# Kernel optimization log

Measured on AMD Instinct MI355X. Metric: run time of the kernel, lower is better.

Reference implementation:

```python
import jax, jax.numpy as jnp
import numpy as np

N, T, C = 4, 2048, 1024
H = 16
D = C // H  # head_dim = 64


def setup_inputs() -> dict:
    key = jax.random.key(0)
    ks = jax.random.split(key, 6)
    s = 1.0 / np.sqrt(C)
    return {
        "x": jax.random.normal(ks[0], (N, T, C), dtype=jnp.float32),
        "Wq": jax.random.normal(ks[1], (C, C), dtype=jnp.float32) * s,
        "Wk": jax.random.normal(ks[2], (C, C), dtype=jnp.float32) * s,
        "Wv": jax.random.normal(ks[3], (C, C), dtype=jnp.float32) * s,
        "Wo": jax.random.normal(ks[4], (C, C), dtype=jnp.float32) * s,
        "bo": jax.random.normal(ks[5], (C,), dtype=jnp.float32) * s,
    }


def reference(x, Wq, Wk, Wv, Wo, bo):
    n, t, c = x.shape
    # torch nn.Linear: y = x @ W.T
    q = (x @ Wq.T).reshape(n, t, H, D).transpose(0, 2, 1, 3)  # [N,H,T,D]
    k = (x @ Wk.T).reshape(n, t, H, D).transpose(0, 2, 1, 3)
    v = (x @ Wv.T).reshape(n, t, H, D).transpose(0, 2, 1, 3)
    # NOTE: module scales by sqrt(embed_dim), not sqrt(head_dim)
    energy = jnp.einsum("nhqd,nhkd->nhqk", q, k) / jnp.sqrt(jnp.float32(c))
    causal = jnp.tril(jnp.ones((t, t), dtype=bool))  # [T,T]
    energy = jnp.where(causal[None, None], energy, -jnp.inf)
    attn = jax.nn.softmax(energy, axis=-1)
    out = jnp.einsum("nhqk,nhkd->nhqd", attn, v)  # [N,H,T,D]
    out = out.transpose(0, 2, 1, 3).reshape(n, t, c)
    return out @ Wo.T + bo
```

## Files before the change

### kernel.cpp

```cpp
#include <hip/hip_runtime.h>
#include <math.h>

#define N_ 4
#define T_ 2048
#define C_ 1024
#define H_ 16
#define D_ 64
#define NTC (N_*T_*C_)
#define WELEM (C_*C_)

typedef float f32x4  __attribute__((ext_vector_type(4)));
typedef float f32x16 __attribute__((ext_vector_type(16)));
typedef short bf16x8 __attribute__((ext_vector_type(8)));

static __device__ __forceinline__ unsigned short f2bf(float f) {
    union { float f; unsigned u; } v; v.f = f;
    unsigned r = v.u + 0x7FFFu + ((v.u >> 16) & 1u);
    return (unsigned short)(r >> 16);
}

static __device__ __forceinline__ unsigned cvtpk(float lo, float hi) {
    unsigned r;
    asm("v_cvt_pk_bf16_f32 %0, %1, %2" : "=v"(r) : "v"(lo), "v"(hi));
    return r;
}
#define PLSWAP(a, b) asm("v_permlane32_swap_b32 %0, %1" : "+v"(a), "+v"(b))

#define GLDS16(gptr, lptr) \
    __builtin_amdgcn_global_load_lds((const __attribute__((address_space(1))) void*)(gptr), \
                                     (__attribute__((address_space(3))) void*)(lptr), 16, 0, 0)

__global__ __launch_bounds__(256) void cast_x(const float* __restrict__ src,
                                              unsigned short* __restrict__ dst) {
    const int i = blockIdx.x * 256 + threadIdx.x;
    const float4 a = ((const float4*)src)[i * 2];
    const float4 b = ((const float4*)src)[i * 2 + 1];
    unsigned short u[8] = {f2bf(a.x), f2bf(a.y), f2bf(a.z), f2bf(a.w),
                           f2bf(b.x), f2bf(b.y), f2bf(b.z), f2bf(b.w)};
    *(uint4*)&dst[(size_t)i * 8] = *(const uint4*)u;
}

__global__ __launch_bounds__(256) void cast_w4(const float* __restrict__ w0,
                                               const float* __restrict__ w1,
                                               const float* __restrict__ w2,
                                               const float* __restrict__ w3,
                                               unsigned short* __restrict__ dst) {
    const int z = blockIdx.y;
    const float* __restrict__ src = (z == 0) ? w0 : (z == 1) ? w1 : (z == 2) ? w2 : w3;
    unsigned short* __restrict__ d = dst + (size_t)z * WELEM;
    const int i = blockIdx.x * 256 + threadIdx.x;
    const float4 a = ((const float4*)src)[i * 2];
    const float4 b = ((const float4*)src)[i * 2 + 1];
    unsigned short u[8] = {f2bf(a.x), f2bf(a.y), f2bf(a.z), f2bf(a.w),
                           f2bf(b.x), f2bf(b.y), f2bf(b.z), f2bf(b.w)};
    *(uint4*)&d[(size_t)i * 8] = *(const uint4*)u;
}

#define GEMM_BODY(Aptr, Bptr)                                                           \
    __shared__ __align__(16) unsigned short Abuf[128 * 32];                             \
    __shared__ __align__(16) unsigned short Bbuf[128 * 32];                             \
    const int tid  = threadIdx.x;                                                       \
    const int lane = tid & 63;                                                          \
    const int w    = tid >> 6;                                                          \
    const int lo   = lane & 15;                                                         \
    const int hi   = lane >> 4;                                                         \
    const int wm   = w >> 1;                                                            \
    const int wn   = w & 1;                                                             \
    const int rowBase = blockIdx.x * 128;                                               \
    const int colBase = blockIdx.y * 128;                                               \
    f32x4 acc[4][4];                                                                    \
    _Pragma("unroll")                                                                   \
    for (int i = 0; i < 4; ++i)                                                         \
        _Pragma("unroll")                                                               \
        for (int j = 0; j < 4; ++j) acc[i][j] = (f32x4)(0.f);                           \
    const int i0 = tid, i1 = tid + 256;                                                 \
    const int r0 = i0 >> 2, s0_ = i0 & 3, g0 = s0_ ^ ((r0 >> 1) & 3);                   \
    const int r1 = i1 >> 2, s1_ = i1 & 3, g1 = s1_ ^ ((r1 >> 1) & 3);                   \
    const unsigned short* gA0 = (Aptr) + (size_t)(rowBase + r0) * C_ + g0 * 8;          \
    const unsigned short* gA1 = (Aptr) + (size_t)(rowBase + r1) * C_ + g1 * 8;          \
    const unsigned short* gB0 = (Bptr) + (size_t)(colBase + r0) * C_ + g0 * 8;          \
    const unsigned short* gB1 = (Bptr) + (size_t)(colBase + r1) * C_ + g1 * 8;          \
    for (int k0 = 0; k0 < C_; k0 += 32) {                                               \
        GLDS16(gA0 + k0, &Abuf[i0 * 8]);                                                \
        GLDS16(gA1 + k0, &Abuf[i1 * 8]);                                                \
        GLDS16(gB0 + k0, &Bbuf[i0 * 8]);                                                \
        GLDS16(gB1 + k0, &Bbuf[i1 * 8]);                                                \
        __syncthreads();                                                                \
        bf16x8 af[4], bfv[4];                                                           \
        _Pragma("unroll")                                                               \
        for (int mi = 0; mi < 4; ++mi) {                                                \
            const int row = wm * 64 + mi * 16 + lo;                                     \
            const int slot = hi ^ ((row >> 1) & 3);                                     \
            af[mi] = *(const bf16x8*)&Abuf[row * 32 + slot * 8];                        \
        }                                                                               \
        _Pragma("unroll")                                                               \
        for (int ni = 0; ni < 4; ++ni) {                                                \
            const int row = wn * 64 + ni * 16 + lo;                                     \
            const int slot = hi ^ ((row >> 1) & 3);                                     \
            bfv[ni] = *(const bf16x8*)&Bbuf[row * 32 + slot * 8];                       \
        }                                                                               \
        _Pragma("unroll")                                                               \
        for (int mi = 0; mi < 4; ++mi)                                                  \
            _Pragma("unroll")                                                           \
            for (int ni = 0; ni < 4; ++ni)                                              \
                acc[mi][ni] = __builtin_amdgcn_mfma_f32_16x16x32_bf16(af[mi], bfv[ni],  \
                                                                     acc[mi][ni], 0, 0, 0); \
        __syncthreads();                                                                \
    }

__global__ __launch_bounds__(256) void qkv_fused(const unsigned short* __restrict__ A,
                                                 const unsigned short* __restrict__ Wall,
                                                 unsigned short* __restrict__ qkvout) {
    const int z = blockIdx.z;
    const unsigned short* __restrict__ B = Wall + (size_t)z * WELEM;
    unsigned short* __restrict__ Y = qkvout + (size_t)z * NTC;
    const float oscale = (z == 0) ? (0.03125f * 1.44269504f) : 1.0f;

    GEMM_BODY(A, B)

    if (z < 2) {
        #pragma unroll
        for (int mi = 0; mi < 4; ++mi) {
            #pragma unroll
            for (int r = 0; r < 4; ++r) {
                const int row = rowBase + wm * 64 + mi * 16 + hi * 4 + r;
                const int nn = row >> 11, tt = row & (T_ - 1);
                #pragma unroll
                for (int ni = 0; ni < 4; ++ni) {
                    const int col = colBase + wn * 64 + ni * 16 + lo;
                    Y[((size_t)((nn * H_ + (col >> 6)) * T_ + tt)) * D_ + (col & 63)] =
                        f2bf(acc[mi][ni][r] * oscale);
                }
            }
        }
    } else {
        #pragma unroll
        for (int mi = 0; mi < 4; ++mi) {
            #pragma unroll
            for (int r = 0; r < 4; ++r) {
                const int row = rowBase + wm * 64 + mi * 16 + hi * 4 + r;
                const int nn = row >> 11, tt = row & (T_ - 1);
                #pragma unroll
                for (int ni = 0; ni < 4; ++ni) {
                    const int col = colBase + wn * 64 + ni * 16 + lo;
                    Y[(size_t)((nn * 16 + (col >> 6)) * 64 + (col & 63)) * T_ + tt] =
                        f2bf(acc[mi][ni][r]);
                }
            }
        }
    }
}

__global__ __launch_bounds__(256) void out_gemm(const unsigned short* __restrict__ A,
                                                const unsigned short* __restrict__ B,
                                                const float* __restrict__ bo,
                                                float* __restrict__ out) {
    GEMM_BODY(A, B)

    float bias[4];
    #pragma unroll
    for (int ni = 0; ni < 4; ++ni) bias[ni] = bo[colBase + wn * 64 + ni * 16 + lo];
    #pragma unroll
    for (int mi = 0; mi < 4; ++mi) {
        #pragma unroll
        for (int r = 0; r < 4; ++r) {
            const int row = rowBase + wm * 64 + mi * 16 + hi * 4 + r;
            #pragma unroll
            for (int ni = 0; ni < 4; ++ni) {
                const int col = colBase + wn * 64 + ni * 16 + lo;
                out[(size_t)row * C_ + col] = acc[mi][ni][r] + bias[ni];
            }
        }
    }
}

__global__ __launch_bounds__(256, 2) void attn_mfma(const unsigned short* __restrict__ qg,
                                                    const unsigned short* __restrict__ kg,
                                                    const unsigned short* __restrict__ vtg,
                                                    unsigned short* __restrict__ ob) {
    __shared__ __align__(16) unsigned short Kt[2][64 * 64];
    __shared__ __align__(16) unsigned short Vt[2][64 * 64];

    const int tid  = threadIdx.x;
    const int w    = tid >> 6;
    const int lane = tid & 63;
    const int ql   = lane & 31;
    const int h    = lane >> 5;
    const int bid  = blockIdx.x;
    const int qtile = 15 - (bid >> 6);
    const int nh   = bid & 63;
    const int qb   = qtile * 128;
    const size_t base  = (size_t)nh * (T_ * D_);
    const size_t vbase = (size_t)nh * 64 * T_;
    const int qrow0 = qb + w * 32;

    bf16x8 qf[4];
    #pragma unroll
    for (int dsl = 0; dsl < 4; ++dsl)
        qf[dsl] = *(const bf16x8*)(qg + base + (size_t)(qrow0 + ql) * D_ + dsl * 16 + h * 8);

    f32x16 acc0 = (f32x16)(0.f), acc1 = (f32x16)(0.f);
    float mrun = -INFINITY, lrun = 0.f;

    const int mynkt  = (qrow0 >> 6) + 1;
    const int nktmax = (qb >> 6) + 2;
    const int csubdiag = (w & 1) + 1;

    const int i0 = tid, i1 = tid + 256;
    const int kr0 = i0 >> 3, kc0 = ((i0 & 7) ^ (kr0 & 7)) * 8;
    const int kr1 = i1 >> 3, kc1 = ((i1 & 7) ^ (kr1 & 7)) * 8;

    #define STAGE(kt_, buf_)                                                            \
        do {                                                                            \
            const int kb_ = (kt_) * 64;                                                 \
            GLDS16(kg + base + (size_t)(kb_ + kr0) * D_ + kc0, &Kt[buf_][i0 * 8]);      \
            GLDS16(kg + base + (size_t)(kb_ + kr1) * D_ + kc1, &Kt[buf_][i1 * 8]);      \
            GLDS16(vtg + vbase + (size_t)kr0 * T_ + kb_ + kc0, &Vt[buf_][i0 * 8]);      \
            GLDS16(vtg + vbase + (size_t)kr1 * T_ + kb_ + kc1, &Vt[buf_][i1 * 8]);      \
        } while (0)

    STAGE(0, 0);
    __syncthreads();
    int cur = 0;

    for (int kt = 0; kt < nktmax; ++kt) {
        if (kt + 1 < nktmax) STAGE(kt + 1, cur ^ 1);

        if (kt < mynkt) {
            const bool diag = (kt == mynkt - 1);
            const int csub = diag ? csubdiag : 2;
            const unsigned short* Kb = Kt[cur];
            const unsigned short* Vb = Vt[cur];

            f32x16 s0, s1;
            __builtin_amdgcn_s_setprio(1);
            {
                f32x16 z = (f32x16)(0.f);
                #pragma unroll
                for (int dsl = 0; dsl < 4; ++dsl) {
                    const bf16x8 ka = *(const bf16x8*)&Kb[ql * 64 + ((dsl * 2 + h) ^ (ql & 7)) * 8];
                    z = __builtin_amdgcn_mfma_f32_32x32x16_bf16(ka, qf[dsl], z, 0, 0, 0);
                }
                s0 = z;
            }
            if (csub > 1) {
                f32x16 z = (f32x16)(0.f);
                #pragma unroll
                for (int dsl = 0; dsl < 4; ++dsl) {
                    const bf16x8 ka = *(const bf16x8*)&Kb[(32 + ql) * 64 + ((dsl * 2 + h) ^ (ql & 7)) * 8];
                    z = __builtin_amdgcn_mfma_f32_32x32x16_bf16(ka, qf[dsl], z, 0, 0, 0);
                }
                s1 = z;
            }
            __builtin_amdgcn_s_setprio(0);

            if (diag) {
                #pragma unroll
                for (int r = 0; r < 16; ++r) {
                    const int rc = (r & 3) + 8 * (r >> 2) + 4 * h;
                    if (csub == 1) { if (rc > ql) s0[r] = -1e30f; }
                    else           { if (rc > ql) s1[r] = -1e30f; }
                }
            }

            float tm = fmaxf(s0[0], s0[1]);
            #pragma unroll
            for (int r = 2; r < 16; r += 2) tm = fmaxf(tm, fmaxf(s0[r], s0[r + 1]));
            if (csub > 1) {
                #pragma unroll
                for (int r = 0; r < 16; r += 2) tm = fmaxf(tm, fmaxf(s1[r], s1[r + 1]));
            }
            tm = fmaxf(tm, __shfl_xor(tm, 32));

            if (!__all(tm <= mrun + 8.f)) {
                const float mnew = fmaxf(mrun, tm);
                const float fsc = exp2f(mrun - mnew);
                mrun = mnew;
                lrun *= fsc;
                #pragma unroll
                for (int r = 0; r < 16; ++r) {
                    const float f = __shfl(fsc, (r & 3) + 8 * (r >> 2) + 4 * h);
                    acc0[r] *= f; acc1[r] *= f;
                }
            }

            float psum = 0.f;
            #pragma unroll
            for (int r = 0; r < 16; ++r) { s0[r] = exp2f(s0[r] - mrun); psum += s0[r]; }
            if (csub > 1) {
                #pragma unroll
                for (int r = 0; r < 16; ++r) { s1[r] = exp2f(s1[r] - mrun); psum += s1[r]; }
            }
            psum += __shfl_xor(psum, 32);
            lrun += psum;

            bf16x8 pa[4];
            #pragma unroll
            for (int a = 0; a < 2; ++a) {
                if (a < csub) {
                    #pragma unroll
                    for (int b = 0; b < 2; ++b) {
                        const f32x16& P = a ? s1 : s0;
                        unsigned w0 = cvtpk(P[8 * b + 0], P[8 * b + 1]);
                        unsigned w1 = cvtpk(P[8 * b + 2], P[8 * b + 3]);
                        unsigned w2 = cvtpk(P[8 * b + 4], P[8 * b + 5]);
                        unsigned w3 = cvtpk(P[8 * b + 6], P[8 * b + 7]);
                        PLSWAP(w0, w2);
                        PLSWAP(w1, w3);
                        unsigned wd[4] = {w0, w1, w2, w3};
                        pa[2 * a + b] = *(bf16x8*)wd;
                    }
                }
            }

            __builtin_amdgcn_s_setprio(1);
            #pragma unroll
            for (int ks = 0; ks < 4; ++ks) {
                if (ks < 2 * csub) {
                    const bf16x8 vf0 = *(const bf16x8*)&Vb[ql * 64 + ((ks * 2 + h) ^ (ql & 7)) * 8];
                    const bf16x8 vf1 = *(const bf16x8*)&Vb[(32 + ql) * 64 + ((ks * 2 + h) ^ (ql & 7)) * 8];
                    acc0 = __builtin_amdgcn_mfma_f32_32x32x16_bf16(pa[ks], vf0, acc0, 0, 0, 0);
                    acc1 = __builtin_amdgcn_mfma_f32_32x32x16_bf16(pa[ks], vf1, acc1, 0, 0, 0);
                }
            }
            __builtin_amdgcn_s_setprio(0);
        }
        __syncthreads();
        cur ^= 1;
    }

    const float linv = 1.f / lrun;
    const int nn = nh >> 4, hh = nh & 15;
    #pragma unroll
    for (int r = 0; r < 16; ++r) {
        const int rc = (r & 3) + 8 * (r >> 2) + 4 * h;
        const float li = __shfl(linv, rc);
        const size_t rb = (size_t)(nn * T_ + qrow0 + rc) * C_ + hh * 64;
        ob[rb + ql]      = f2bf(acc0[r] * li);
        ob[rb + 32 + ql] = f2bf(acc1[r] * li);
    }
    #undef STAGE
}

extern "C" void kernel_launch(void* const* d_in, const int* in_sizes, int n_in,
                              void* d_out, int out_size, void* d_ws, size_t ws_size,
                              hipStream_t stream) {
    const float* x  = (const float*)d_in[0];
    const float* Wq = (const float*)d_in[1];
    const float* Wk = (const float*)d_in[2];
    const float* Wv = (const float*)d_in[3];
    const float* Wo = (const float*)d_in[4];
    const float* bo = (const float*)d_in[5];
    float* out = (float*)d_out;

    unsigned short* ws = (unsigned short*)d_ws;
    unsigned short* x_bf   = ws;
    unsigned short* w_bf   = x_bf + (size_t)NTC;
    unsigned short* qkv_bf = w_bf + (size_t)4 * WELEM;
    unsigned short* a_bf   = qkv_bf + (size_t)3 * NTC;

    cast_x<<<NTC / (8 * 256), 256, 0, stream>>>(x, x_bf);
    dim3 gw(WELEM / (8 * 256), 4);
    cast_w4<<<gw, 256, 0, stream>>>(Wq, Wk, Wv, Wo, w_bf);

    dim3 gq(N_ * T_ / 128, C_ / 128, 3);
    qkv_fused<<<gq, 256, 0, stream>>>(x_bf, w_bf, qkv_bf);

    attn_mfma<<<(T_ / 128) * (N_ * H_), 256, 0, stream>>>(
        qkv_bf, qkv_bf + (size_t)NTC, qkv_bf + (size_t)2 * NTC, a_bf);

    dim3 gg(N_ * T_ / 128, C_ / 128);
    out_gemm<<<gg, 256, 0, stream>>>(a_bf, w_bf + 3 * (size_t)WELEM, bo, out);
}
```

Measured before the change: 182.7 us.

## Raise attention occupancy, interleave causal q-tile order, tree-reduce softmax max/sum

Raises the attention kernel's launch bound from 2 to 4 blocks per CU, asking the compiler to cap registers so more waves can hide latency. Changes the block-to-q-tile mapping so long (late) and short (early) causal tiles are interleaved in groups rather than strictly descending, to balance work across concurrently resident blocks. Rewrites the row-max and row-sum reductions as shallow trees to shorten serial dependency chains. The tighter register budget risks spills in a kernel holding two 16-wide accumulators, fragments and score tiles.

```diff
diff --git a/kernel.cpp b/kernel.cpp
--- a/kernel.cpp
+++ b/kernel.cpp
@@ -174,7 +174,7 @@
     }
 }
 
-__global__ __launch_bounds__(256, 2) void attn_mfma(const unsigned short* __restrict__ qg,
+__global__ __launch_bounds__(256, 4) void attn_mfma(const unsigned short* __restrict__ qg,
                                                     const unsigned short* __restrict__ kg,
                                                     const unsigned short* __restrict__ vtg,
                                                     unsigned short* __restrict__ ob) {
@@ -187,7 +187,10 @@
     const int ql   = lane & 31;
     const int h    = lane >> 5;
     const int bid  = blockIdx.x;
-    const int qtile = 15 - (bid >> 6);
+    const int g    = bid >> 6;
+    const int gi   = g & 3;
+    const int gq   = g >> 2;
+    const int qtile = (gq == 0) ? (15 - gi) : (gq == 1) ? (8 + gi) : (gq == 2) ? (7 - gi) : gi;
     const int nh   = bid & 63;
     const int qb   = qtile * 128;
     const size_t base  = (size_t)nh * (T_ * D_);
@@ -263,14 +266,24 @@
                 }
             }
 
-            float tm = fmaxf(s0[0], s0[1]);
-            #pragma unroll
-            for (int r = 2; r < 16; r += 2) tm = fmaxf(tm, fmaxf(s0[r], s0[r + 1]));
-            if (csub > 1) {
-                #pragma unroll
-                for (int r = 0; r < 16; r += 2) tm = fmaxf(tm, fmaxf(s1[r], s1[r + 1]));
-            }
-            tm = fmaxf(tm, __shfl_xor(tm, 32));
+            float tm;
+            {
+                float t[8];
+                if (csub > 1) {
+                    #pragma unroll
+                    for (int r = 0; r < 8; ++r)
+                        t[r] = fmaxf(fmaxf(s0[2 * r], s0[2 * r + 1]),
+                                     fmaxf(s1[2 * r], s1[2 * r + 1]));
+                } else {
+                    #pragma unroll
+                    for (int r = 0; r < 8; ++r) t[r] = fmaxf(s0[2 * r], s0[2 * r + 1]);
+                }
+                t[0] = fmaxf(t[0], t[4]); t[1] = fmaxf(t[1], t[5]);
+                t[2] = fmaxf(t[2], t[6]); t[3] = fmaxf(t[3], t[7]);
+                t[0] = fmaxf(t[0], t[2]); t[1] = fmaxf(t[1], t[3]);
+                tm = fmaxf(t[0], t[1]);
+                tm = fmaxf(tm, __shfl_xor(tm, 32));
+            }
 
             if (!__all(tm <= mrun + 8.f)) {
                 const float mnew = fmaxf(mrun, tm);
@@ -284,15 +297,28 @@
                 }
             }
 
-            float psum = 0.f;
-            #pragma unroll
-            for (int r = 0; r < 16; ++r) { s0[r] = exp2f(s0[r] - mrun); psum += s0[r]; }
+            #pragma unroll
+            for (int r = 0; r < 16; ++r) s0[r] = exp2f(s0[r] - mrun);
             if (csub > 1) {
                 #pragma unroll
-                for (int r = 0; r < 16; ++r) { s1[r] = exp2f(s1[r] - mrun); psum += s1[r]; }
-            }
-            psum += __shfl_xor(psum, 32);
-            lrun += psum;
+                for (int r = 0; r < 16; ++r) s1[r] = exp2f(s1[r] - mrun);
+            }
+            {
+                float t[8];
+                if (csub > 1) {
+                    #pragma unroll
+                    for (int r = 0; r < 8; ++r)
+                        t[r] = (s0[2 * r] + s0[2 * r + 1]) + (s1[2 * r] + s1[2 * r + 1]);
+                } else {
+                    #pragma unroll
+                    for (int r = 0; r < 8; ++r) t[r] = s0[2 * r] + s0[2 * r + 1];
+                }
+                t[0] += t[4]; t[1] += t[5]; t[2] += t[6]; t[3] += t[7];
+                t[0] += t[2]; t[1] += t[3];
+                float psum = t[0] + t[1];
+                psum += __shfl_xor(psum, 32);
+                lrun += psum;
+            }
 
             bf16x8 pa[4];
             #pragma unroll
```

New measurement: 197.9 us. 8.3% more time.
